# Kernel tuning notes

Measured on AMD Instinct MI355X. Metric: run time of the kernel, lower is better.

The kernel has to match this reference:

```python
import jax, jax.numpy as jnp
import numpy as np

B, S, D = 2, 2048, 1024
E, K, F = 8, 2, 4 * 1024  # num_experts, top_k, fc_rate*embed_dim
T = B * S


def setup_inputs() -> dict:
    key = jax.random.key(0)
    ks = jax.random.split(key, 8)
    w = lambda k, shape: jax.random.normal(k, shape, jnp.float32) * 0.02
    return {
        "hidden_states": jax.random.normal(ks[0], (B, S, D), jnp.float32),
        "noise": jax.random.normal(ks[1], (T, E), jnp.float32),  # randn_like in router
        "Wg": w(ks[2], (D, E)), "bg": jnp.zeros((E,), jnp.float32),
        "Wn": w(ks[3], (D, E)), "bn": jnp.zeros((E,), jnp.float32),
        "W1": w(ks[4], (E, D, F)), "b1": jnp.zeros((E, F), jnp.float32),
        "W2": w(ks[5], (E, F, D)), "b2": jnp.zeros((E, D), jnp.float32),
    }


def reference(hidden_states, noise, Wg, bg, Wn, bn, W1, b1, W2, b2):
    b, s, d = hidden_states.shape
    x = hidden_states.reshape(-1, d)  # [T, D]

    # --- NoisyTopkRouter ---
    gate_logits = x @ Wg + bg                        # [T, E]
    noise_logits = x @ Wn + bn                       # [T, E]
    noisy_logits = gate_logits + noise * jax.nn.softplus(noise_logits)
    rw = jax.nn.softmax(noisy_logits.astype(jnp.float32), axis=-1)
    top_w, top_i = jax.lax.top_k(rw, K)              # [T, K]
    top_w = top_w / top_w.sum(-1, keepdims=True)
    top_w = top_w.astype(x.dtype)

    # Dense per-token combine coefficients: coef[t,e] = sum_k top_w[t,k]*[top_i[t,k]==e]
    tok = jnp.arange(x.shape[0])[:, None]
    coef = jnp.zeros((x.shape[0], E), x.dtype).at[tok, top_i].add(top_w)  # [T, E]

    # --- Experts: Linear -> GELU(exact) -> Linear (dropout = identity, eval mode) ---
    h = jax.nn.gelu(jnp.einsum('td,edf->tef', x, W1) + b1, approximate=False)  # [T,E,F]
    y = jnp.einsum('tef,efd->ted', h, W2) + b2                                  # [T,E,D]
    out = jnp.einsum('ted,te->td', y, coef)                                     # [T,D]

    return out.reshape(b, s, d), noisy_logits, gate_logits
```

## Files before the change

### kernel.cpp

```cpp
#include <hip/hip_runtime.h>
#include <hip/hip_bf16.h>

#define T_TOK 4096
#define D_DIM 1024
#define E_NUM 8
#define F_DIM 4096
#define NPAIR 8192

#define BM 256
#define BN 256
#define BK 64
#define NTMAX 40

typedef float f32x4 __attribute__((ext_vector_type(4)));
typedef __bf16 bf16x8 __attribute__((ext_vector_type(8)));
typedef unsigned short u16x8 __attribute__((ext_vector_type(8)));
typedef unsigned short u16x4 __attribute__((ext_vector_type(4)));

__device__ __forceinline__ unsigned short f2bf(float f) {
    unsigned int u = __float_as_uint(f);
    u += 0x7fffu + ((u >> 16) & 1u);
    return (unsigned short)(u >> 16);
}

typedef const __attribute__((address_space(1))) void GV;
typedef __attribute__((address_space(3))) void LV;

__device__ __forceinline__ void load_lds16(const void* g, void* l) {
    __builtin_amdgcn_global_load_lds((GV*)g, (LV*)l, 16, 0, 0);
}

__device__ __forceinline__ bf16x8 lds_frag(const unsigned short* S, int row, int cs) {
    int byte = row * (BK * 2) + ((cs * 2) ^ ((row & 7) << 4));
    return *(const bf16x8*)((const char*)S + byte);
}

__global__ __launch_bounds__(256) void router_convert_kernel(
    const float* __restrict__ x, const float* __restrict__ noise,
    const float* __restrict__ Wg, const float* __restrict__ bg,
    const float* __restrict__ Wn, const float* __restrict__ bn,
    float* __restrict__ out_noisy, float* __restrict__ out_gate,
    int* __restrict__ tk_idx, float* __restrict__ tk_w,
    unsigned short* __restrict__ xb)
{
    int lane = threadIdx.x & 63;
    int t = blockIdx.x * 4 + (threadIdx.x >> 6);
    const float* xr = x + (size_t)t * D_DIM;
    unsigned short* xbr = xb + (size_t)t * D_DIM;

    #pragma unroll
    for (int r = 0; r < 4; ++r) {
        int d = r * 256 + lane * 4;
        float4 v = *(const float4*)(xr + d);
        u16x4 o;
        o[0] = f2bf(v.x); o[1] = f2bf(v.y); o[2] = f2bf(v.z); o[3] = f2bf(v.w);
        *(u16x4*)(xbr + d) = o;
    }

    float ag[E_NUM] = {}, an[E_NUM] = {};
    for (int it = 0; it < D_DIM / 64; ++it) {
        int d = it * 64 + lane;
        float xv = xr[d];
        float4 g0 = *(const float4*)(Wg + (size_t)d * E_NUM);
        float4 g1 = *(const float4*)(Wg + (size_t)d * E_NUM + 4);
        float4 m0 = *(const float4*)(Wn + (size_t)d * E_NUM);
        float4 m1 = *(const float4*)(Wn + (size_t)d * E_NUM + 4);
        ag[0] += xv * g0.x; ag[1] += xv * g0.y; ag[2] += xv * g0.z; ag[3] += xv * g0.w;
        ag[4] += xv * g1.x; ag[5] += xv * g1.y; ag[6] += xv * g1.z; ag[7] += xv * g1.w;
        an[0] += xv * m0.x; an[1] += xv * m0.y; an[2] += xv * m0.z; an[3] += xv * m0.w;
        an[4] += xv * m1.x; an[5] += xv * m1.y; an[6] += xv * m1.z; an[7] += xv * m1.w;
    }
    #pragma unroll
    for (int off = 32; off > 0; off >>= 1) {
        #pragma unroll
        for (int e = 0; e < E_NUM; ++e) {
            ag[e] += __shfl_xor(ag[e], off);
            an[e] += __shfl_xor(an[e], off);
        }
    }
    if (lane == 0) {
        float nz[E_NUM];
        #pragma unroll
        for (int e = 0; e < E_NUM; ++e) {
            float g = ag[e] + bg[e];
            float nn = an[e] + bn[e];
            float sp = fmaxf(nn, 0.f) + log1pf(expf(-fabsf(nn)));
            float z = g + noise[(size_t)t * E_NUM + e] * sp;
            out_gate[(size_t)t * E_NUM + e] = g;
            out_noisy[(size_t)t * E_NUM + e] = z;
            nz[e] = z;
        }
        int e0 = 0;
        #pragma unroll
        for (int e = 1; e < E_NUM; ++e) if (nz[e] > nz[e0]) e0 = e;
        int e1 = (e0 == 0) ? 1 : 0;
        #pragma unroll
        for (int e = 0; e < E_NUM; ++e) if (e != e0 && nz[e] > nz[e1]) e1 = e;
        float b = expf(nz[e1] - nz[e0]);
        float w0 = 1.f / (1.f + b);
        float w1 = b / (1.f + b);
        tk_idx[t * 2] = e0;  tk_idx[t * 2 + 1] = e1;
        tk_w[t * 2] = w0;    tk_w[t * 2 + 1] = w1;
    }
}

__global__ __launch_bounds__(256) void scan_scatter_kernel(
    const int* __restrict__ tk_idx,
    int* __restrict__ perm, int* __restrict__ meta)
{
    __shared__ int cnt[256][E_NUM];
    __shared__ int soff[E_NUM];
    int tid = threadIdx.x;
    const int PPT = NPAIR / 256;
    int p0 = tid * PPT;

    int c[E_NUM] = {};
    for (int i = 0; i < PPT; ++i) c[tk_idx[p0 + i]]++;
    #pragma unroll
    for (int e = 0; e < E_NUM; ++e) cnt[tid][e] = c[e];
    __syncthreads();

    if (tid < E_NUM) {
        int s = 0;
        for (int j = 0; j < 256; ++j) { int v = cnt[j][tid]; cnt[j][tid] = s; s += v; }
        soff[tid] = s;
    }
    __syncthreads();

    if (tid == 0) {
        int off = 0, nt = 0;
        for (int e = 0; e < E_NUM; ++e) {
            int ce = soff[e];
            meta[1 + e] = off;
            meta[9 + e] = ce;
            for (int j = 0; j < ce; j += BM) {
                meta[32 + nt]  = e;
                meta[160 + nt] = off + j;
                meta[288 + nt] = off + ce;
                nt++;
            }
            off += ce;
        }
        meta[0] = nt;
    }
    __syncthreads();
    if (tid < E_NUM) soff[tid] = meta[1 + tid];
    __syncthreads();

    int pos[E_NUM];
    #pragma unroll
    for (int e = 0; e < E_NUM; ++e) pos[e] = soff[e] + cnt[tid][e];
    for (int i = 0; i < PPT; ++i) {
        int e = tk_idx[p0 + i];
        perm[pos[e]++] = p0 + i;
    }
}

__global__ __launch_bounds__(256) void transpose_kernel(
    const float* __restrict__ W, unsigned short* __restrict__ WT, int R, int C)
{
    __shared__ float tile[64][65];
    int e = blockIdx.z;
    int c0 = blockIdx.x * 64, r0 = blockIdx.y * 64;
    int tx = threadIdx.x & 15, ty = threadIdx.x >> 4;
    const float* src = W + (size_t)e * R * C;
    #pragma unroll
    for (int j = 0; j < 4; ++j) {
        int r = ty + 16 * j;
        float4 v = *(const float4*)(src + (size_t)(r0 + r) * C + c0 + tx * 4);
        *(float4*)&tile[r][tx * 4] = v;
    }
    __syncthreads();
    unsigned short* dst = WT + (size_t)e * C * R;
    int sx = threadIdx.x & 7, sy = threadIdx.x >> 3;
    #pragma unroll
    for (int j = 0; j < 2; ++j) {
        int c = sy + 32 * j;
        u16x8 o;
        #pragma unroll
        for (int k = 0; k < 8; ++k) o[k] = f2bf(tile[sx * 8 + k][c]);
        *(u16x8*)(dst + (size_t)(c0 + c) * R + r0 + sx * 8) = o;
    }
}

#define GEMM_COMPUTE() do {                                                                \
    _Pragma("unroll")                                                                      \
    for (int kk = 0; kk < BK; kk += 32) {                                                  \
        bf16x8 af[4], bf[4];                                                               \
        _Pragma("unroll")                                                                  \
        for (int m_ = 0; m_ < 4; ++m_)                                                     \
            af[m_] = lds_frag(As, wm + m_ * 16 + (lane & 15), kk + (lane >> 4) * 8);       \
        _Pragma("unroll")                                                                  \
        for (int n_ = 0; n_ < 4; ++n_)                                                     \
            bf[n_] = lds_frag(Bs, wn + n_ * 16 + (lane & 15), kk + (lane >> 4) * 8);       \
        _Pragma("unroll")                                                                  \
        for (int m_ = 0; m_ < 4; ++m_)                                                     \
            _Pragma("unroll")                                                              \
            for (int n_ = 0; n_ < 4; ++n_)                                                 \
                acc[m_][n_] = __builtin_amdgcn_mfma_f32_16x16x32_bf16(af[m_], bf[n_],      \
                                                                      acc[m_][n_], 0, 0, 0); \
    }                                                                                      \
} while (0)

__global__ __launch_bounds__(1024, 4) void fc1_kernel(
    const unsigned short* __restrict__ xb,
    const unsigned short* __restrict__ W1T,
    const float* __restrict__ b1,
    const int* __restrict__ perm,
    const int* __restrict__ meta,
    unsigned short* __restrict__ h)
{
    const int nwg = NTMAX * 16;
    int bid = blockIdx.x;
    int wg = (bid & 7) * (nwg >> 3) + (bid >> 3);
    int tile = wg >> 4;
    int n0 = (wg & 15) * BN;
    if (tile >= meta[0]) return;
    int e    = meta[32 + tile];
    int rs   = meta[160 + tile];
    int rend = meta[288 + tile];

    __shared__ __align__(16) unsigned short As[BM * BK];
    __shared__ __align__(16) unsigned short Bs[BN * BK];

    int tid = threadIdx.x, lane = tid & 63, wv = tid >> 6;
    int wm = (wv >> 2) * 64, wn = (wv & 3) * 64;
    int s = tid & 7;

    const unsigned short* asrc[2];
    const unsigned short* bsrc[2];
    #pragma unroll
    for (int i = 0; i < 2; ++i) {
        int row = (tid >> 3) + i * 128;
        int csw = (s ^ (row & 7)) * 8;
        int pos = rs + row; if (pos >= NPAIR) pos = NPAIR - 1;
        int tt = perm[pos] >> 1;
        asrc[i] = xb + (size_t)tt * D_DIM + csw;
        bsrc[i] = W1T + ((size_t)e * F_DIM + n0 + row) * D_DIM + csw;
    }

    f32x4 acc[4][4] = {};

    const int NT = D_DIM / BK;
    for (int t = 0; t < NT; ++t) {
        int k0 = t * BK;
        #pragma unroll
        for (int i = 0; i < 2; ++i) {
            load_lds16(asrc[i] + k0, &As[(tid + i * 1024) * 8]);
            load_lds16(bsrc[i] + k0, &Bs[(tid + i * 1024) * 8]);
        }
        asm volatile("s_waitcnt vmcnt(0)" ::: "memory");
        __builtin_amdgcn_s_barrier();
        __builtin_amdgcn_s_setprio(1);
        GEMM_COMPUTE();
        __builtin_amdgcn_s_setprio(0);
        asm volatile("s_waitcnt lgkmcnt(0)" ::: "memory");
        __builtin_amdgcn_s_barrier();
    }

    #pragma unroll
    for (int m = 0; m < 4; ++m) {
        #pragma unroll
        for (int j = 0; j < 4; ++j) {
            int r = wm + m * 16 + (lane >> 4) * 4 + j;
            int pos = rs + r;
            if (pos >= rend) continue;
            #pragma unroll
            for (int n = 0; n < 4; ++n) {
                int col = n0 + wn + n * 16 + (lane & 15);
                float v = acc[m][n][j] + b1[e * F_DIM + col];
                v = 0.5f * v * (1.f + erff(v * 0.70710678118654752f));
                h[(size_t)pos * F_DIM + col] = f2bf(v);
            }
        }
    }
}

__global__ __launch_bounds__(1024, 4) void fc2_kernel(
    const unsigned short* __restrict__ h,
    const unsigned short* __restrict__ W2T,
    const float* __restrict__ b2,
    const int* __restrict__ perm,
    const float* __restrict__ tk_w,
    const int* __restrict__ meta,
    float* __restrict__ out)
{
    const int nwg = NTMAX * 8;
    int bid = blockIdx.x;
    int wg = (bid & 7) * (nwg >> 3) + (bid >> 3);
    int tile = wg >> 3;
    int rem  = wg & 7;
    int n0 = (rem >> 1) * BN;
    int ks = rem & 1;
    if (tile >= meta[0]) return;
    int e    = meta[32 + tile];
    int rs   = meta[160 + tile];
    int rend = meta[288 + tile];
    int kbeg = ks * (F_DIM / 2);

    __shared__ __align__(16) unsigned short As[BM * BK];
    __shared__ __align__(16) unsigned short Bs[BN * BK];

    int tid = threadIdx.x, lane = tid & 63, wv = tid >> 6;
    int wm = (wv >> 2) * 64, wn = (wv & 3) * 64;
    int s = tid & 7;

    const unsigned short* asrc[2];
    const unsigned short* bsrc[2];
    #pragma unroll
    for (int i = 0; i < 2; ++i) {
        int row = (tid >> 3) + i * 128;
        int csw = (s ^ (row & 7)) * 8;
        int pos = rs + row; if (pos >= NPAIR) pos = NPAIR - 1;
        asrc[i] = h + (size_t)pos * F_DIM + kbeg + csw;
        bsrc[i] = W2T + ((size_t)e * D_DIM + n0 + row) * F_DIM + kbeg + csw;
    }

    f32x4 acc[4][4] = {};

    const int NT = (F_DIM / 2) / BK;
    for (int t = 0; t < NT; ++t) {
        int k0 = t * BK;
        #pragma unroll
        for (int i = 0; i < 2; ++i) {
            load_lds16(asrc[i] + k0, &As[(tid + i * 1024) * 8]);
            load_lds16(bsrc[i] + k0, &Bs[(tid + i * 1024) * 8]);
        }
        asm volatile("s_waitcnt vmcnt(0)" ::: "memory");
        __builtin_amdgcn_s_barrier();
        __builtin_amdgcn_s_setprio(1);
        GEMM_COMPUTE();
        __builtin_amdgcn_s_setprio(0);
        asm volatile("s_waitcnt lgkmcnt(0)" ::: "memory");
        __builtin_amdgcn_s_barrier();
    }

    #pragma unroll
    for (int m = 0; m < 4; ++m) {
        #pragma unroll
        for (int j = 0; j < 4; ++j) {
            int r = wm + m * 16 + (lane >> 4) * 4 + j;
            int pos = rs + r;
            if (pos >= rend) continue;
            int pr = perm[pos];
            int t2 = pr >> 1;
            float w = tk_w[pr];
            #pragma unroll
            for (int n = 0; n < 4; ++n) {
                int col = n0 + wn + n * 16 + (lane & 15);
                float base = (ks == 0) ? b2[e * D_DIM + col] : 0.f;
                float v = (acc[m][n][j] + base) * w;
                atomicAdd(&out[(size_t)t2 * D_DIM + col], v);
            }
        }
    }
}

extern "C" void kernel_launch(void* const* d_in, const int* in_sizes, int n_in,
                              void* d_out, int out_size, void* d_ws, size_t ws_size,
                              hipStream_t stream)
{
    const float* x     = (const float*)d_in[0];
    const float* noise = (const float*)d_in[1];
    const float* Wg    = (const float*)d_in[2];
    const float* bg    = (const float*)d_in[3];
    const float* Wn    = (const float*)d_in[4];
    const float* bn    = (const float*)d_in[5];
    const float* W1    = (const float*)d_in[6];
    const float* b1    = (const float*)d_in[7];
    const float* W2    = (const float*)d_in[8];
    const float* b2    = (const float*)d_in[9];

    float* out       = (float*)d_out;
    float* out_noisy = out + (size_t)T_TOK * D_DIM;
    float* out_gate  = out_noisy + (size_t)T_TOK * E_NUM;

    char* ws = (char*)d_ws;
    int*   tk_idx = (int*)ws;
    float* tk_w   = (float*)(ws + 32768);
    int*   perm   = (int*)(ws + 65536);
    int*   meta   = (int*)(ws + 98304);
    size_t off = 131072;
    unsigned short* xb   = (unsigned short*)(ws + off); off += (size_t)T_TOK * D_DIM * 2;
    unsigned short* W1T  = (unsigned short*)(ws + off); off += (size_t)E_NUM * F_DIM * D_DIM * 2;
    unsigned short* W2T  = (unsigned short*)(ws + off); off += (size_t)E_NUM * D_DIM * F_DIM * 2;
    unsigned short* hbuf = (unsigned short*)(ws + off); off += (size_t)NPAIR * F_DIM * 2;

    hipMemsetAsync(d_out, 0, (size_t)out_size * sizeof(float), stream);

    router_convert_kernel<<<T_TOK / 4, 256, 0, stream>>>(x, noise, Wg, bg, Wn, bn,
                                                         out_noisy, out_gate, tk_idx, tk_w, xb);
    scan_scatter_kernel<<<1, 256, 0, stream>>>(tk_idx, perm, meta);
    transpose_kernel<<<dim3(D_DIM / 64, F_DIM / 64, E_NUM), 256, 0, stream>>>(W2, W2T, F_DIM, D_DIM);
    transpose_kernel<<<dim3(F_DIM / 64, D_DIM / 64, E_NUM), 256, 0, stream>>>(W1, W1T, D_DIM, F_DIM);

    fc1_kernel<<<NTMAX * 16, 1024, 0, stream>>>(xb, W1T, b1, perm, meta, hbuf);
    fc2_kernel<<<NTMAX * 8, 1024, 0, stream>>>(hbuf, W2T, b2, perm, tk_w, meta, out);
}
```

Baseline: 501.2 us.

## Double-buffer GEMM tiles with BK=32 and persistent XCD-partitioned grid

```diff
diff --git a/kernel.cpp b/kernel.cpp
--- a/kernel.cpp
+++ b/kernel.cpp
@@ -9,8 +9,7 @@
 
 #define BM 256
 #define BN 256
-#define BK 64
-#define NTMAX 40
+#define BK 32
 
 typedef float f32x4 __attribute__((ext_vector_type(4)));
 typedef __bf16 bf16x8 __attribute__((ext_vector_type(8)));
@@ -30,8 +29,10 @@
     __builtin_amdgcn_global_load_lds((GV*)g, (LV*)l, 16, 0, 0);
 }
 
-__device__ __forceinline__ bf16x8 lds_frag(const unsigned short* S, int row, int cs) {
-    int byte = row * (BK * 2) + ((cs * 2) ^ ((row & 7) << 4));
+__device__ __forceinline__ int swz4(int r) { return (r ^ (r >> 2)) & 3; }
+
+__device__ __forceinline__ bf16x8 lds_frag32(const unsigned short* S, int row, int cb) {
+    int byte = row * 64 + ((cb ^ swz4(row)) << 4);
     return *(const bf16x8*)((const char*)S + byte);
 }
 
@@ -183,22 +184,38 @@
     }
 }
 
-#define GEMM_COMPUTE() do {                                                                \
+#define GEMM_COMPUTE(Abuf, Bbuf) do {                                                      \
+    bf16x8 af[4], bf[4];                                                                   \
     _Pragma("unroll")                                                                      \
-    for (int kk = 0; kk < BK; kk += 32) {                                                  \
-        bf16x8 af[4], bf[4];                                                               \
-        _Pragma("unroll")                                                                  \
-        for (int m_ = 0; m_ < 4; ++m_)                                                     \
-            af[m_] = lds_frag(As, wm + m_ * 16 + (lane & 15), kk + (lane >> 4) * 8);       \
+    for (int m_ = 0; m_ < 4; ++m_)                                                         \
+        af[m_] = lds_frag32((Abuf), wm + m_ * 16 + (lane & 15), lane >> 4);                \
+    _Pragma("unroll")                                                                      \
+    for (int n_ = 0; n_ < 4; ++n_)                                                         \
+        bf[n_] = lds_frag32((Bbuf), wn + n_ * 16 + (lane & 15), lane >> 4);                \
+    _Pragma("unroll")                                                                      \
+    for (int m_ = 0; m_ < 4; ++m_)                                                         \
         _Pragma("unroll")                                                                  \
         for (int n_ = 0; n_ < 4; ++n_)                                                     \
-            bf[n_] = lds_frag(Bs, wn + n_ * 16 + (lane & 15), kk + (lane >> 4) * 8);       \
-        _Pragma("unroll")                                                                  \
-        for (int m_ = 0; m_ < 4; ++m_)                                                     \
-            _Pragma("unroll")                                                              \
-            for (int n_ = 0; n_ < 4; ++n_)                                                 \
-                acc[m_][n_] = __builtin_amdgcn_mfma_f32_16x16x32_bf16(af[m_], bf[n_],      \
-                                                                      acc[m_][n_], 0, 0, 0); \
+            acc[m_][n_] = __builtin_amdgcn_mfma_f32_16x16x32_bf16(af[m_], bf[n_],          \
+                                                                  acc[m_][n_], 0, 0, 0);  \
+} while (0)
+
+#define GEMM_LOOP(NT, STAGE) do {                                                          \
+    STAGE(0, 0);                                                                           \
+    for (int t = 0; t < (NT); ++t) {                                                       \
+        int cbuf = t & 1;                                                                  \
+        if (t + 1 < (NT)) {                                                                \
+            STAGE((t + 1) * BK, cbuf ^ 1);                                                 \
+            asm volatile("s_waitcnt vmcnt(2)" ::: "memory");                               \
+        } else {                                                                           \
+            asm volatile("s_waitcnt vmcnt(0)" ::: "memory");                               \
+        }                                                                                  \
+        __builtin_amdgcn_s_barrier();                                                      \
+        __builtin_amdgcn_s_setprio(1);                                                     \
+        GEMM_COMPUTE(As[cbuf], Bs[cbuf]);                                                  \
+        __builtin_amdgcn_s_setprio(0);                                                     \
+        asm volatile("s_waitcnt lgkmcnt(0)" ::: "memory");                                 \
+        __builtin_amdgcn_s_barrier();                                                      \
     }                                                                                      \
 } while (0)
 
@@ -210,69 +227,62 @@
     const int* __restrict__ meta,
     unsigned short* __restrict__ h)
 {
-    const int nwg = NTMAX * 16;
-    int bid = blockIdx.x;
-    int wg = (bid & 7) * (nwg >> 3) + (bid >> 3);
-    int tile = wg >> 4;
-    int n0 = (wg & 15) * BN;
-    if (tile >= meta[0]) return;
-    int e    = meta[32 + tile];
-    int rs   = meta[160 + tile];
-    int rend = meta[288 + tile];
-
-    __shared__ __align__(16) unsigned short As[BM * BK];
-    __shared__ __align__(16) unsigned short Bs[BN * BK];
+    __shared__ __align__(16) unsigned short As[2][BM * BK];
+    __shared__ __align__(16) unsigned short Bs[2][BN * BK];
+
+    int nt = meta[0];
+    int total = nt * 16;
+    int ipx = (total + 7) >> 3;
+    int xcd = blockIdx.x & 7;
+    int slot = blockIdx.x >> 3;
+    int lim = (xcd + 1) * ipx; if (lim > total) lim = total;
 
     int tid = threadIdx.x, lane = tid & 63, wv = tid >> 6;
     int wm = (wv >> 2) * 64, wn = (wv & 3) * 64;
-    int s = tid & 7;
-
-    const unsigned short* asrc[2];
-    const unsigned short* bsrc[2];
-    #pragma unroll
-    for (int i = 0; i < 2; ++i) {
-        int row = (tid >> 3) + i * 128;
-        int csw = (s ^ (row & 7)) * 8;
-        int pos = rs + row; if (pos >= NPAIR) pos = NPAIR - 1;
-        int tt = perm[pos] >> 1;
-        asrc[i] = xb + (size_t)tt * D_DIM + csw;
-        bsrc[i] = W1T + ((size_t)e * F_DIM + n0 + row) * D_DIM + csw;
-    }
-
-    f32x4 acc[4][4] = {};
-
-    const int NT = D_DIM / BK;
-    for (int t = 0; t < NT; ++t) {
-        int k0 = t * BK;
-        #pragma unroll
-        for (int i = 0; i < 2; ++i) {
-            load_lds16(asrc[i] + k0, &As[(tid + i * 1024) * 8]);
-            load_lds16(bsrc[i] + k0, &Bs[(tid + i * 1024) * 8]);
-        }
-        asm volatile("s_waitcnt vmcnt(0)" ::: "memory");
-        __builtin_amdgcn_s_barrier();
-        __builtin_amdgcn_s_setprio(1);
-        GEMM_COMPUTE();
-        __builtin_amdgcn_s_setprio(0);
-        asm volatile("s_waitcnt lgkmcnt(0)" ::: "memory");
-        __builtin_amdgcn_s_barrier();
-    }
-
-    #pragma unroll
-    for (int m = 0; m < 4; ++m) {
-        #pragma unroll
-        for (int j = 0; j < 4; ++j) {
-            int r = wm + m * 16 + (lane >> 4) * 4 + j;
-            int pos = rs + r;
-            if (pos >= rend) continue;
+    int row_st = wv * 16 + (lane >> 2);
+    int slot_st = lane & 3;
+    int csw = ((slot_st ^ swz4(row_st)) * 8);
+    unsigned short* ldsA = &As[0][0] + wv * 512 + lane * 8;
+    unsigned short* ldsB = &Bs[0][0] + wv * 512 + lane * 8;
+
+    for (int item = xcd * ipx + slot; item < lim; item += 32) {
+        int tile = item >> 4;
+        int n0 = (item & 15) * BN;
+        int e    = meta[32 + tile];
+        int rs   = meta[160 + tile];
+        int rend = meta[288 + tile];
+
+        int pos = rs + row_st; if (pos >= NPAIR) pos = NPAIR - 1;
+        const unsigned short* aptr = xb + (size_t)(perm[pos] >> 1) * D_DIM + csw;
+        const unsigned short* bptr = W1T + ((size_t)e * F_DIM + n0 + row_st) * D_DIM + csw;
+
+        f32x4 acc[4][4] = {};
+
+#define STAGE1(k0, b) do {                                         \
+    load_lds16(aptr + (k0), ldsA + (b) * (BM * BK));               \
+    load_lds16(bptr + (k0), ldsB + (b) * (BN * BK));               \
+} while (0)
+
+        GEMM_LOOP(D_DIM / BK, STAGE1);
+#undef STAGE1
+
+        #pragma unroll
+        for (int m = 0; m < 4; ++m) {
             #pragma unroll
-            for (int n = 0; n < 4; ++n) {
-                int col = n0 + wn + n * 16 + (lane & 15);
-                float v = acc[m][n][j] + b1[e * F_DIM + col];
-                v = 0.5f * v * (1.f + erff(v * 0.70710678118654752f));
-                h[(size_t)pos * F_DIM + col] = f2bf(v);
+            for (int j = 0; j < 4; ++j) {
+                int r = wm + m * 16 + (lane >> 4) * 4 + j;
+                int p = rs + r;
+                if (p >= rend) continue;
+                #pragma unroll
+                for (int n = 0; n < 4; ++n) {
+                    int col = n0 + wn + n * 16 + (lane & 15);
+                    float v = acc[m][n][j] + b1[e * F_DIM + col];
+                    v = 0.5f * v * (1.f + erff(v * 0.70710678118654752f));
+                    h[(size_t)p * F_DIM + col] = f2bf(v);
+                }
             }
         }
+        __builtin_amdgcn_s_barrier();
     }
 }
 
@@ -285,74 +295,68 @@
     const int* __restrict__ meta,
     float* __restrict__ out)
 {
-    const int nwg = NTMAX * 8;
-    int bid = blockIdx.x;
-    int wg = (bid & 7) * (nwg >> 3) + (bid >> 3);
-    int tile = wg >> 3;
-    int rem  = wg & 7;
-    int n0 = (rem >> 1) * BN;
-    int ks = rem & 1;
-    if (tile >= meta[0]) return;
-    int e    = meta[32 + tile];
-    int rs   = meta[160 + tile];
-    int rend = meta[288 + tile];
-    int kbeg = ks * (F_DIM / 2);
-
-    __shared__ __align__(16) unsigned short As[BM * BK];
-    __shared__ __align__(16) unsigned short Bs[BN * BK];
+    __shared__ __align__(16) unsigned short As[2][BM * BK];
+    __shared__ __align__(16) unsigned short Bs[2][BN * BK];
+
+    int nt = meta[0];
+    int total = nt * 8;
+    int ipx = (total + 7) >> 3;
+    int xcd = blockIdx.x & 7;
+    int slot = blockIdx.x >> 3;
+    int lim = (xcd + 1) * ipx; if (lim > total) lim = total;
 
     int tid = threadIdx.x, lane = tid & 63, wv = tid >> 6;
     int wm = (wv >> 2) * 64, wn = (wv & 3) * 64;
-    int s = tid & 7;
-
-    const unsigned short* asrc[2];
-    const unsigned short* bsrc[2];
-    #pragma unroll
-    for (int i = 0; i < 2; ++i) {
-        int row = (tid >> 3) + i * 128;
-        int csw = (s ^ (row & 7)) * 8;
-        int pos = rs + row; if (pos >= NPAIR) pos = NPAIR - 1;
-        asrc[i] = h + (size_t)pos * F_DIM + kbeg + csw;
-        bsrc[i] = W2T + ((size_t)e * D_DIM + n0 + row) * F_DIM + kbeg + csw;
-    }
-
-    f32x4 acc[4][4] = {};
-
-    const int NT = (F_DIM / 2) / BK;
-    for (int t = 0; t < NT; ++t) {
-        int k0 = t * BK;
-        #pragma unroll
-        for (int i = 0; i < 2; ++i) {
-            load_lds16(asrc[i] + k0, &As[(tid + i * 1024) * 8]);
-            load_lds16(bsrc[i] + k0, &Bs[(tid + i * 1024) * 8]);
-        }
-        asm volatile("s_waitcnt vmcnt(0)" ::: "memory");
-        __builtin_amdgcn_s_barrier();
-        __builtin_amdgcn_s_setprio(1);
-        GEMM_COMPUTE();
-        __builtin_amdgcn_s_setprio(0);
-        asm volatile("s_waitcnt lgkmcnt(0)" ::: "memory");
-        __builtin_amdgcn_s_barrier();
-    }
-
-    #pragma unroll
-    for (int m = 0; m < 4; ++m) {
-        #pragma unroll
-        for (int j = 0; j < 4; ++j) {
-            int r = wm + m * 16 + (lane >> 4) * 4 + j;
-            int pos = rs + r;
-            if (pos >= rend) continue;
-            int pr = perm[pos];
-            int t2 = pr >> 1;
-            float w = tk_w[pr];
+    int row_st = wv * 16 + (lane >> 2);
+    int slot_st = lane & 3;
+    int csw = ((slot_st ^ swz4(row_st)) * 8);
+    unsigned short* ldsA = &As[0][0] + wv * 512 + lane * 8;
+    unsigned short* ldsB = &Bs[0][0] + wv * 512 + lane * 8;
+
+    for (int item = xcd * ipx + slot; item < lim; item += 32) {
+        int tile = item >> 3;
+        int rem  = item & 7;
+        int n0 = (rem >> 1) * BN;
+        int ks = rem & 1;
+        int kbeg = ks * (F_DIM / 2);
+        int e    = meta[32 + tile];
+        int rs   = meta[160 + tile];
+        int rend = meta[288 + tile];
+
+        int pos = rs + row_st; if (pos >= NPAIR) pos = NPAIR - 1;
+        const unsigned short* aptr = h + (size_t)pos * F_DIM + kbeg + csw;
+        const unsigned short* bptr = W2T + ((size_t)e * D_DIM + n0 + row_st) * F_DIM + kbeg + csw;
+
+        f32x4 acc[4][4] = {};
+
+#define STAGE2(k0, b) do {                                         \
+    load_lds16(aptr + (k0), ldsA + (b) * (BM * BK));               \
+    load_lds16(bptr + (k0), ldsB + (b) * (BN * BK));               \
+} while (0)
+
+        GEMM_LOOP((F_DIM / 2) / BK, STAGE2);
+#undef STAGE2
+
+        #pragma unroll
+        for (int m = 0; m < 4; ++m) {
             #pragma unroll
-            for (int n = 0; n < 4; ++n) {
-                int col = n0 + wn + n * 16 + (lane & 15);
-                float base = (ks == 0) ? b2[e * D_DIM + col] : 0.f;
-                float v = (acc[m][n][j] + base) * w;
-                atomicAdd(&out[(size_t)t2 * D_DIM + col], v);
+            for (int j = 0; j < 4; ++j) {
+                int r = wm + m * 16 + (lane >> 4) * 4 + j;
+                int p = rs + r;
+                if (p >= rend) continue;
+                int pr = perm[p];
+                int t2 = pr >> 1;
+                float w = tk_w[pr];
+                #pragma unroll
+                for (int n = 0; n < 4; ++n) {
+                    int col = n0 + wn + n * 16 + (lane & 15);
+                    float base = (ks == 0) ? b2[e * D_DIM + col] : 0.f;
+                    float v = (acc[m][n][j] + base) * w;
+                    atomicAdd(&out[(size_t)t2 * D_DIM + col], v);
+                }
             }
         }
+        __builtin_amdgcn_s_barrier();
     }
 }
 
@@ -394,6 +398,6 @@
     transpose_kernel<<<dim3(D_DIM / 64, F_DIM / 64, E_NUM), 256, 0, stream>>>(W2, W2T, F_DIM, D_DIM);
     transpose_kernel<<<dim3(F_DIM / 64, D_DIM / 64, E_NUM), 256, 0, stream>>>(W1, W1T, D_DIM, F_DIM);
 
-    fc1_kernel<<<NTMAX * 16, 1024, 0, stream>>>(xb, W1T, b1, perm, meta, hbuf);
-    fc2_kernel<<<NTMAX * 8, 1024, 0, stream>>>(hbuf, W2T, b2, perm, tk_w, meta, out);
-}
+    fc1_kernel<<<256, 1024, 0, stream>>>(xb, W1T, b1, perm, meta, hbuf);
+    fc2_kernel<<<256, 1024, 0, stream>>>(hbuf, W2T, b2, perm, tk_w, meta, out);
+}
```

After: 480.5 us. 4.1% less time.
